# Optimization experiments

Measured on AMD Instinct MI355X. Metric: run time of the kernel, lower is better.

## Reference

```python
import jax, jax.numpy as jnp
import numpy as np

# ---- config (from Mamba2Config defaults) ----
D_MODEL = 1024
D_STATE = 128
D_CONV = 4
EXPAND = 2
HEADDIM = 64
D_INNER = EXPAND * D_MODEL          # 2048
NHEADS = D_INNER // HEADDIM         # 32
CONV_DIM = D_INNER + 2 * D_STATE    # 2304 (ngroups=1)
D_IN_PROJ = 2 * D_INNER + 2 * D_STATE + NHEADS  # 4384
INTER = ((int(D_MODEL * 8 / 3) + 63) // 64) * 64  # 2752
EPS = 1e-6
BATCH, SEQLEN = 2, 1024


def rmsnorm(x, w):
    return x * jax.lax.rsqrt(jnp.mean(x * x, axis=-1, keepdims=True) + EPS) * w


def setup_inputs() -> dict:
    key = jax.random.key(0)
    ks = jax.random.split(key, 16)
    s = 0.02
    return {
        "hidden_states": jax.random.normal(ks[0], (BATCH, SEQLEN, D_MODEL), jnp.float32),
        "norm_w": jnp.ones((D_MODEL,), jnp.float32),
        "in_proj_w": jax.random.normal(ks[1], (D_IN_PROJ, D_MODEL), jnp.float32) * s,
        "conv_w": jax.random.normal(ks[2], (CONV_DIM, D_CONV), jnp.float32) * 0.2,
        "conv_b": jnp.zeros((CONV_DIM,), jnp.float32),
        "dt_bias": jax.random.normal(ks[3], (NHEADS,), jnp.float32) * 0.5,
        "A_log": jnp.log(jax.random.uniform(ks[4], (NHEADS,), jnp.float32, 1.0, 16.0)),
        "D": jnp.ones((NHEADS,), jnp.float32) + jax.random.normal(ks[5], (NHEADS,), jnp.float32) * 0.05,
        "ssm_norm_w": jnp.ones((D_INNER,), jnp.float32),
        "out_proj_w": jax.random.normal(ks[6], (D_MODEL, D_INNER), jnp.float32) * s,
        "post_norm_w": jnp.ones((D_MODEL,), jnp.float32),
        "gate_w": jax.random.normal(ks[7], (INTER, D_MODEL), jnp.float32) * s,
        "up_w": jax.random.normal(ks[8], (INTER, D_MODEL), jnp.float32) * s,
        "down_w": jax.random.normal(ks[9], (D_MODEL, INTER), jnp.float32) * s,
    }


def _mixer(u, in_proj_w, conv_w, conv_b, dt_bias, A_log, D, ssm_norm_w, out_proj_w):
    b, l, _ = u.shape
    zxbcdt = u @ in_proj_w.T                              # (b,l,4384)
    z = zxbcdt[..., :D_INNER]                             # gate
    xBC = zxbcdt[..., D_INNER:D_INNER + CONV_DIM]
    dt = zxbcdt[..., -NHEADS:]

    # causal depthwise conv1d (kernel D_CONV) + SiLU
    xp = jnp.pad(xBC, ((0, 0), (D_CONV - 1, 0), (0, 0)))
    xBC = sum(xp[:, k:k + l, :] * conv_w[:, k] for k in range(D_CONV)) + conv_b
    xBC = jax.nn.silu(xBC)

    xs = xBC[..., :D_INNER].reshape(b, l, NHEADS, HEADDIM)   # (b,l,h,p)
    Bm = xBC[..., D_INNER:D_INNER + D_STATE]                  # (b,l,n)
    Cm = xBC[..., -D_STATE:]                                  # (b,l,n)

    dt = jax.nn.softplus(dt + dt_bias)                        # (b,l,h)
    A = -jnp.exp(A_log)                                       # (h,)

    def step(h, inp):
        dt_t, x_t, B_t, C_t = inp                             # (b,h),(b,h,p),(b,n),(b,n)
        dA = jnp.exp(dt_t * A)                                # (b,h)
        h = h * dA[..., None, None] + jnp.einsum('bh,bhp,bn->bhpn', dt_t, x_t, B_t)
        y_t = jnp.einsum('bhpn,bn->bhp', h, C_t)
        return h, y_t

    h0 = jnp.zeros((b, NHEADS, HEADDIM, D_STATE), u.dtype)
    xsT = (jnp.moveaxis(dt, 1, 0), jnp.moveaxis(xs, 1, 0),
           jnp.moveaxis(Bm, 1, 0), jnp.moveaxis(Cm, 1, 0))
    _, yT = jax.lax.scan(step, h0, xsT)                       # (l,b,h,p)
    y = jnp.moveaxis(yT, 0, 1) + D[None, None, :, None] * xs  # skip term
    y = y.reshape(b, l, D_INNER)

    # gated RMSNorm (norm_before_gate=False): normalize y*silu(z)
    y = rmsnorm(y * jax.nn.silu(z), ssm_norm_w)
    return y @ out_proj_w.T


def reference(hidden_states, norm_w, in_proj_w, conv_w, conv_b, dt_bias, A_log, D,
              ssm_norm_w, out_proj_w, post_norm_w, gate_w, up_w, down_w):
    res = hidden_states
    h = rmsnorm(hidden_states, norm_w)
    h = _mixer(h, in_proj_w, conv_w, conv_b, dt_bias, A_log, D, ssm_norm_w, out_proj_w)
    x = res + h
    res = x
    h = rmsnorm(x, post_norm_w)
    h = (jax.nn.silu(h @ gate_w.T) * (h @ up_w.T)) @ down_w.T  # SwiGLU MLP
    return res + h
```

## Files before the change

### kernel.cpp

```cpp
#include <hip/hip_runtime.h>
#include <hip/hip_bf16.h>

#define SEQLEN   1024
#define NTOK     2048
#define DMODEL   1024
#define DSTATE   128
#define DINNER   2048
#define NHEADS   32
#define HEADDIM  64
#define CONVDIM  2304
#define DINPROJ  4384
#define INTER    2752
#define Q        64
#define NCHUNK   16

typedef __hip_bfloat16 bf16;
typedef unsigned short ushort_t;
typedef __attribute__((ext_vector_type(8))) short bf16x8;
typedef __attribute__((ext_vector_type(4))) float f32x4;
typedef __attribute__((ext_vector_type(4))) unsigned short u16x4;

__device__ __forceinline__ float bf2f(bf16 x) { return __bfloat162float(x); }
__device__ __forceinline__ float bfu2f(ushort_t u) {
    return __uint_as_float(((unsigned)u) << 16);
}
__device__ __forceinline__ ushort_t f2bfu(float x) {
    union { bf16 h; ushort_t u; } c; c.h = __float2bfloat16(x); return c.u;
}

__device__ __forceinline__ void glds16(const void* g, void* l) {
    __builtin_amdgcn_global_load_lds(
        (const __attribute__((address_space(1))) void*)g,
        (__attribute__((address_space(3))) void*)l, 16, 0, 0);
}

template <int N>
__device__ __forceinline__ void pipe_fence() {
    if constexpr (N == 4)
        asm volatile("s_waitcnt vmcnt(4) lgkmcnt(0)" ::: "memory");
    else if constexpr (N == 2)
        asm volatile("s_waitcnt vmcnt(2) lgkmcnt(0)" ::: "memory");
    else
        asm volatile("s_waitcnt vmcnt(0) lgkmcnt(0)" ::: "memory");
    __builtin_amdgcn_s_barrier();
    __builtin_amdgcn_sched_barrier(0);
}

__device__ inline float block_reduce_sum(float v) {
    __shared__ float red[4];
    #pragma unroll
    for (int off = 32; off >= 1; off >>= 1) v += __shfl_down(v, off);
    int lane = threadIdx.x & 63, w = threadIdx.x >> 6;
    if (lane == 0) red[w] = v;
    __syncthreads();
    return red[0] + red[1] + red[2] + red[3];
}

__global__ __launch_bounds__(256) void f2bf_kernel(
    const float* __restrict__ src, ushort_t* __restrict__ dst, int n)
{
    const int i = (blockIdx.x * 256 + threadIdx.x) * 4;
    if (i < n) {
        const f32x4 v = *(const f32x4*)(src + i);
        u16x4 o;
        #pragma unroll
        for (int k = 0; k < 4; k++) o[k] = f2bfu(v[k]);
        *(u16x4*)(dst + i) = o;
    }
}

#define NWOP (DMODEL * DINNER)
#define NWG  (INTER * DMODEL)
__global__ __launch_bounds__(256) void convert_weights_kernel(
    const float* __restrict__ wop, const float* __restrict__ wg,
    const float* __restrict__ wu, const float* __restrict__ wd,
    ushort_t* __restrict__ dWop, ushort_t* __restrict__ dWgu,
    ushort_t* __restrict__ dWdn)
{
    const int i4 = (blockIdx.x * 256 + threadIdx.x) * 4;
    const float* src;
    ushort_t* dst;
    if (i4 < NWOP) { src = wop + i4; dst = dWop + i4; }
    else if (i4 < NWOP + NWG) {
        const int e = i4 - NWOP, row = e >> 10, col = e & 1023;
        src = wg + e; dst = dWgu + ((size_t)(2 * row) << 10) + col;
    } else if (i4 < NWOP + 2 * NWG) {
        const int e = i4 - NWOP - NWG, row = e >> 10, col = e & 1023;
        src = wu + e; dst = dWgu + ((size_t)(2 * row + 1) << 10) + col;
    } else if (i4 < NWOP + 3 * NWG) {
        const int e = i4 - NWOP - 2 * NWG;
        src = wd + e; dst = dWdn + e;
    } else return;
    const f32x4 v = *(const f32x4*)src;
    u16x4 o;
    #pragma unroll
    for (int k = 0; k < 4; k++) o[k] = f2bfu(v[k]);
    *(u16x4*)dst = o;
}

__global__ __launch_bounds__(256) void rmsnorm1024_kernel(
    const float* __restrict__ x, const float* __restrict__ w, bf16* __restrict__ out)
{
    const int token = blockIdx.x, t = threadIdx.x;
    float v[4]; float ss = 0.f;
    #pragma unroll
    for (int i = 0; i < 4; i++) {
        v[i] = x[(size_t)token * DMODEL + t * 4 + i];
        ss += v[i] * v[i];
    }
    ss = block_reduce_sum(ss);
    const float scale = rsqrtf(ss * (1.0f / DMODEL) + 1e-6f);
    #pragma unroll
    for (int i = 0; i < 4; i++)
        out[(size_t)token * DMODEL + t * 4 + i] =
            __float2bfloat16(v[i] * scale * w[t * 4 + i]);
}

template <int EPI, int MT, int NT>
__global__ __launch_bounds__(256) void gemm_bf(
    const bf16* __restrict__ A, const bf16* __restrict__ W,
    float* __restrict__ Cf, const float* __restrict__ resid_f,
    bf16* __restrict__ out_bf, int M, int N, int K)
{
    __shared__ ushort_t As[3][MT * 32];
    __shared__ ushort_t Bs[3][NT * 32];
    const int tid = threadIdx.x;
    const int w = tid >> 6, lane = tid & 63;
    constexpr int NLD = MT / 64 + NT / 64;

    const int gdx = gridDim.x, gdy = gridDim.y;
    const int nwg = gdx * gdy;
    const int orig = blockIdx.x + gdx * blockIdx.y;
    const int q8 = nwg >> 3, r8 = nwg & 7;
    const int xcd = orig & 7, lin = orig >> 3;
    const int wg = (xcd < r8 ? xcd * (q8 + 1) : r8 * (q8 + 1) + (xcd - r8) * q8) + lin;
    const int m0 = (wg % gdy) * MT;
    const int n0 = (wg / gdy) * NT;

    const int srow = tid >> 2;
    const int scol = (((tid & 3) ^ ((srow >> 1) & 3)) * 8);
    const bf16* Agp[MT / 64];
    const bf16* Wgp[NT / 64];
    #pragma unroll
    for (int i = 0; i < MT / 64; i++)
        Agp[i] = A + (size_t)(m0 + i * 64 + srow) * K + scol;
    #pragma unroll
    for (int i = 0; i < NT / 64; i++) {
        const int nr = n0 + i * 64 + srow;
        Wgp[i] = W + (size_t)(nr < N ? nr : 0) * K + scol;
    }

    const int wy = w >> 1, wx = w & 1;
    const int fr = lane & 15;
    const int fq = lane >> 4;
    const int cxor = (fr >> 1) & 3;
    constexpr int MI = MT / 32;
    constexpr int NJ = NT / 32;
    f32x4 acc[MI][NJ];
    #pragma unroll
    for (int i = 0; i < MI; i++)
        #pragma unroll
        for (int j = 0; j < NJ; j++)
            acc[i][j] = (f32x4){0.f, 0.f, 0.f, 0.f};

    const int nk = K >> 5;

    #define STAGE(buf, koff) do {                                         \
        ushort_t* sa_ = &As[buf][w * 512];                                \
        ushort_t* sb_ = &Bs[buf][w * 512];                                \
        _Pragma("unroll")                                                 \
        for (int i_ = 0; i_ < MT / 64; i_++)                              \
            glds16(Agp[i_] + (koff), sa_ + i_ * 2048);                    \
        _Pragma("unroll")                                                 \
        for (int i_ = 0; i_ < NT / 64; i_++)                              \
            glds16(Wgp[i_] + (koff), sb_ + i_ * 2048);                    \
    } while (0)

    STAGE(0, 0);
    STAGE(1, 32);
    pipe_fence<NLD>();

    int cur = 0, stg = 2;
    for (int kt = 0; kt < nk; ++kt) {
        const bool pf = (kt + 2 < nk);
        if (pf) STAGE(stg, (kt + 2) << 5);
        const ushort_t* ca = As[cur];
        const ushort_t* cb = Bs[cur];
        bf16x8 af[MI], bfv[NJ];
        #pragma unroll
        for (int i = 0; i < MI; i++) {
            const int r = wy * (MT / 2) + i * 16 + fr;
            af[i] = *(const bf16x8*)&ca[r * 32 + ((fq ^ cxor) * 8)];
        }
        #pragma unroll
        for (int j = 0; j < NJ; j++) {
            const int r = wx * (NT / 2) + j * 16 + fr;
            bfv[j] = *(const bf16x8*)&cb[r * 32 + ((fq ^ cxor) * 8)];
        }
        #pragma unroll
        for (int i = 0; i < MI; i++)
            #pragma unroll
            for (int j = 0; j < NJ; j++)
                acc[i][j] = __builtin_amdgcn_mfma_f32_16x16x32_bf16(
                    af[i], bfv[j], acc[i][j], 0, 0, 0);
        if (pf)               pipe_fence<NLD>();
        else if (kt + 1 < nk) pipe_fence<0>();
        cur = (cur == 2) ? 0 : cur + 1;
        stg = (stg == 2) ? 0 : stg + 1;
    }
    #undef STAGE

    #pragma unroll
    for (int i = 0; i < MI; i++) {
        #pragma unroll
        for (int j = 0; j < NJ; j++) {
            const int mb = m0 + wy * (MT / 2) + i * 16 + (lane >> 4) * 4;
            const int nn = n0 + wx * (NT / 2) + j * 16 + (lane & 15);
            if (nn < N) {
                #pragma unroll
                for (int r = 0; r < 4; r++) {
                    if (EPI == 2) {
                        const float g = acc[i][j][r];
                        const float u = __shfl_xor(g, 1);
                        if (!(lane & 1)) {
                            const float a = (g / (1.f + expf(-g))) * u;
                            out_bf[(size_t)(mb + r) * (N / 2) + (nn >> 1)] =
                                __float2bfloat16(a);
                        }
                    } else {
                        const size_t idx = (size_t)(mb + r) * N + nn;
                        float v = acc[i][j][r];
                        if (EPI == 1) v += resid_f[idx];
                        Cf[idx] = v;
                    }
                }
            }
        }
    }
}

__global__ __launch_bounds__(256) void gemm_bf_s(
    const bf16* __restrict__ A, const bf16* __restrict__ W,
    float* __restrict__ Cf, const float* __restrict__ resid_f,
    int M, int N, int K)
{
    constexpr int MT = 64, NT = 64;
    __shared__ ushort_t As[2][MT * 64];
    __shared__ ushort_t Bs[2][NT * 64];
    const int tid = threadIdx.x;
    const int w = tid >> 6, lane = tid & 63;

    const int gdx = gridDim.x, gdy = gridDim.y;
    const int nwg = gdx * gdy;
    const int orig = blockIdx.x + gdx * blockIdx.y;
    const int q8 = nwg >> 3, r8 = nwg & 7;
    const int xcd = orig & 7, lin = orig >> 3;
    const int wg = (xcd < r8 ? xcd * (q8 + 1) : r8 * (q8 + 1) + (xcd - r8) * q8) + lin;
    const int m0 = (wg % gdy) * MT;
    const int n0 = (wg / gdy) * NT;

    const int srow = tid >> 3;
    const int scol = (((tid & 7) ^ (srow & 7)) * 8);
    const bf16* Agp[2];
    const bf16* Wgp[2];
    #pragma unroll
    for (int i = 0; i < 2; i++)
        Agp[i] = A + (size_t)(m0 + i * 32 + srow) * K + scol;
    #pragma unroll
    for (int i = 0; i < 2; i++) {
        const int nr = n0 + i * 32 + srow;
        Wgp[i] = W + (size_t)(nr < N ? nr : 0) * K + scol;
    }

    const int wy = w >> 1, wx = w & 1;
    const int fr = lane & 15;
    const int fq = lane >> 4;
    f32x4 acc[2][2];
    #pragma unroll
    for (int i = 0; i < 2; i++)
        #pragma unroll
        for (int j = 0; j < 2; j++)
            acc[i][j] = (f32x4){0.f, 0.f, 0.f, 0.f};

    const int nk = K >> 6;

    #define STAGE_S(buf, koff) do {                                       \
        ushort_t* sa_ = &As[buf][w * 512];                                \
        ushort_t* sb_ = &Bs[buf][w * 512];                                \
        _Pragma("unroll")                                                 \
        for (int i_ = 0; i_ < 2; i_++)                                    \
            glds16(Agp[i_] + (koff), sa_ + i_ * 2048);                    \
        _Pragma("unroll")                                                 \
        for (int i_ = 0; i_ < 2; i_++)                                    \
            glds16(Wgp[i_] + (koff), sb_ + i_ * 2048);                    \
    } while (0)

    STAGE_S(0, 0);
    __syncthreads();

    for (int kt = 0; kt < nk; ++kt) {
        const int cur = kt & 1;
        if (kt + 1 < nk) STAGE_S(cur ^ 1, (kt + 1) << 6);
        const ushort_t* ca = As[cur];
        const ushort_t* cb = Bs[cur];
        #pragma unroll
        for (int ks = 0; ks < 2; ks++) {
            bf16x8 af[2], bfv[2];
            #pragma unroll
            for (int i = 0; i < 2; i++) {
                const int r = wy * 32 + i * 16 + fr;
                const int g = ks * 4 + fq;
                af[i] = *(const bf16x8*)&ca[r * 64 + ((g ^ (r & 7)) * 8)];
            }
            #pragma unroll
            for (int j = 0; j < 2; j++) {
                const int r = wx * 32 + j * 16 + fr;
                const int g = ks * 4 + fq;
                bfv[j] = *(const bf16x8*)&cb[r * 64 + ((g ^ (r & 7)) * 8)];
            }
            #pragma unroll
            for (int i = 0; i < 2; i++)
                #pragma unroll
                for (int j = 0; j < 2; j++)
                    acc[i][j] = __builtin_amdgcn_mfma_f32_16x16x32_bf16(
                        af[i], bfv[j], acc[i][j], 0, 0, 0);
        }
        __syncthreads();
    }
    #undef STAGE_S

    #pragma unroll
    for (int i = 0; i < 2; i++) {
        #pragma unroll
        for (int j = 0; j < 2; j++) {
            const int mb = m0 + wy * 32 + i * 16 + (lane >> 4) * 4;
            const int nn = n0 + wx * 32 + j * 16 + (lane & 15);
            if (nn < N) {
                #pragma unroll
                for (int r = 0; r < 4; r++) {
                    const size_t idx = (size_t)(mb + r) * N + nn;
                    Cf[idx] = acc[i][j][r] + resid_f[idx];
                }
            }
        }
    }
}

#define NCONVBLK ((NTOK * CONVDIM / 4) / 256)
__global__ __launch_bounds__(256) void conv_silu_dt_kernel(
    const float* __restrict__ zx, const float* __restrict__ cw,
    const float* __restrict__ cb, const float* __restrict__ dtbias,
    ushort_t* __restrict__ out, float* __restrict__ dtb_out)
{
    const int bid = blockIdx.x;
    if (bid < NCONVBLK) {
        const int i = bid * 256 + threadIdx.x;
        const int cg = i % (CONVDIM / 4);
        const int token = i / (CONVDIM / 4);
        const int c0 = cg * 4;
        const int l = token & (SEQLEN - 1);
        float a[4];
        #pragma unroll
        for (int j = 0; j < 4; j++) a[j] = cb[c0 + j];
        f32x4 cwv[4];
        #pragma unroll
        for (int j = 0; j < 4; j++) cwv[j] = *(const f32x4*)(cw + (c0 + j) * 4);
        #pragma unroll
        for (int k = 0; k < 4; k++) {
            const int ls = l - 3 + k;
            if (ls >= 0) {
                const f32x4 v = *(const f32x4*)(
                    zx + (size_t)(token - 3 + k) * DINPROJ + DINNER + c0);
                #pragma unroll
                for (int j = 0; j < 4; j++) a[j] += v[j] * cwv[j][k];
            }
        }
        u16x4 o;
        #pragma unroll
        for (int j = 0; j < 4; j++)
            o[j] = f2bfu(a[j] / (1.f + expf(-a[j])));
        *(u16x4*)(out + (size_t)token * CONVDIM + c0) = o;
    } else {
        const int idx = (bid - NCONVBLK) * 256 + threadIdx.x;
        const int h = idx & (NHEADS - 1);
        const int token = idx >> 5;
        float v = zx[(size_t)token * DINPROJ + (DINNER + CONVDIM) + h] + dtbias[h];
        dtb_out[idx] = (v > 20.f) ? v : log1pf(expf(v));
    }
}

__global__ __launch_bounds__(256) void chunk_state_kernel(
    const ushort_t* __restrict__ cvb, const float* __restrict__ dtb,
    const float* __restrict__ A_log, float* __restrict__ ccum,
    ushort_t* __restrict__ Sbuf)
{
    const int bx = blockIdx.x;
    const int bh = bx >> 4, c = bx & 15;
    const int b = bh >> 5, h = bh & 31;
    const int t = threadIdx.x;
    const int w = t >> 6, lane = t & 63;
    const int wy = w >> 1, wx = w & 1;
    const int fr = lane & 15, fk = (lane >> 4) * 8, cr = (lane >> 4) * 4;
    const int tok0 = b * SEQLEN + c * Q;
    const float A = -expf(A_log[h]);

    __shared__ ushort_t sXT[64 * 88];
    __shared__ ushort_t sBT[128 * 88];
    __shared__ float sW[64];

    if (t < 64) {
        const float d = dtb[(size_t)(tok0 + t) * NHEADS + h];
        float s = d;
        #pragma unroll
        for (int off = 1; off < 64; off <<= 1) {
            const float up = __shfl_up(s, off);
            if (t >= off) s += up;
        }
        const float total = __shfl(s, 63);
        sW[t] = expf(A * (total - s)) * d;
        if (t == 63) ccum[bh * NCHUNK + c] = A * total;
    }
    __syncthreads();

    for (int i = t; i < 64 * 64; i += 256) {
        const int l = i >> 6, p = i & 63;
        const float v = bfu2f(cvb[(size_t)(tok0 + l) * CONVDIM + h * HEADDIM + p]);
        sXT[p * 88 + l] = f2bfu(sW[l] * v);
    }
    for (int i = t; i < 128 * 64; i += 256) {
        const int l = i >> 7, n = i & 127;
        sBT[n * 88 + l] = cvb[(size_t)(tok0 + l) * CONVDIM + DINNER + n];
    }
    __syncthreads();

    f32x4 acc[2][4];
    #pragma unroll
    for (int i = 0; i < 2; i++)
        #pragma unroll
        for (int j = 0; j < 4; j++)
            acc[i][j] = (f32x4){0.f, 0.f, 0.f, 0.f};
    #pragma unroll
    for (int k0 = 0; k0 < 64; k0 += 32) {
        bf16x8 af[2], bfv[4];
        #pragma unroll
        for (int i = 0; i < 2; i++)
            af[i] = *(const bf16x8*)&sXT[(wy * 32 + i * 16 + fr) * 88 + fk + k0];
        #pragma unroll
        for (int j = 0; j < 4; j++)
            bfv[j] = *(const bf16x8*)&sBT[(wx * 64 + j * 16 + fr) * 88 + fk + k0];
        #pragma unroll
        for (int i = 0; i < 2; i++)
            #pragma unroll
            for (int j = 0; j < 4; j++)
                acc[i][j] = __builtin_amdgcn_mfma_f32_16x16x32_bf16(
                    af[i], bfv[j], acc[i][j], 0, 0, 0);
    }
    const size_t slot = (size_t)(bh * NCHUNK + c) * 64 * 128;
    #pragma unroll
    for (int i = 0; i < 2; i++) {
        #pragma unroll
        for (int j = 0; j < 4; j++) {
            #pragma unroll
            for (int r = 0; r < 4; r++) {
                const int pr = wy * 32 + i * 16 + cr + r;
                const int nn = wx * 64 + j * 16 + fr;
                Sbuf[slot + pr * 128 + nn] = f2bfu(acc[i][j][r]);
            }
        }
    }
}

__global__ __launch_bounds__(256) void stitch_kernel(
    const float* __restrict__ ccum, ushort_t* __restrict__ Sbuf)
{
    const int bh = blockIdx.x >> 2, ng = blockIdx.x & 3;
    const int t = threadIdx.x, p = t >> 2, q = t & 3;
    float H[8];
    #pragma unroll
    for (int j = 0; j < 8; j++) H[j] = 0.f;
    for (int c = 0; c < NCHUNK; c++) {
        const float P = expf(ccum[bh * NCHUNK + c]);
        const size_t slot = ((size_t)(bh * NCHUNK + c) * 64 + p) * 128 + ng * 32;
        #pragma unroll
        for (int jj = 0; jj < 2; jj++) {
            const u16x4 sv4 = *(const u16x4*)&Sbuf[slot + q * 4 + 16 * jj];
            u16x4 hv4;
            #pragma unroll
            for (int k = 0; k < 4; k++) hv4[k] = f2bfu(H[jj * 4 + k]);
            *(u16x4*)&Sbuf[slot + q * 4 + 16 * jj] = hv4;
            #pragma unroll
            for (int k = 0; k < 4; k++)
                H[jj * 4 + k] = P * H[jj * 4 + k] + bfu2f(sv4[k]);
        }
    }
}

__global__ __launch_bounds__(256) void chunk_scan_mfma_kernel(
    const ushort_t* __restrict__ cvb, const float* __restrict__ dtb,
    const float* __restrict__ A_log, const float* __restrict__ Dh,
    const ushort_t* __restrict__ Sbuf, bf16* __restrict__ ybuf)
{
    const int bx = blockIdx.x;
    const int bh = bx >> 4, c = bx & 15;
    const int b = bh >> 5, h = bh & 31;
    const int t = threadIdx.x;
    const int w = t >> 6, lane = t & 63;
    const int wy = w >> 1, wx = w & 1;
    const int fr = lane & 15;
    const int fk = (lane >> 4) * 8;
    const int cr = (lane >> 4) * 4;
    const int tok0 = b * SEQLEN + c * Q;
    const float A = -expf(A_log[h]);
    const float Dv = Dh[h];

    __shared__ ushort_t sB[64 * 136];
    __shared__ ushort_t sC[64 * 136];
    __shared__ ushort_t sH[64 * 136];
    __shared__ ushort_t sXT[64 * 72];
    __shared__ ushort_t sM[64 * 72];
    __shared__ float    sCum[64];
    __shared__ float    sDtv[64];

    for (int i = t; i < 64 * 32; i += 256) {
        const int row = i >> 5, col = (i & 31) * 4;
        const size_t base = (size_t)(tok0 + row) * CONVDIM;
        *(u16x4*)&sB[row * 136 + col] = *(const u16x4*)&cvb[base + DINNER + col];
        *(u16x4*)&sC[row * 136 + col] = *(const u16x4*)&cvb[base + DINNER + DSTATE + col];
    }
    for (int i = t; i < 64 * 32; i += 256) {
        const int p = i >> 5, l0 = (i & 31) * 2;
        const ushort_t x0 = cvb[(size_t)(tok0 + l0)     * CONVDIM + h * HEADDIM + p];
        const ushort_t x1 = cvb[(size_t)(tok0 + l0 + 1) * CONVDIM + h * HEADDIM + p];
        *(unsigned*)&sXT[p * 72 + l0] = ((unsigned)x1 << 16) | x0;
    }
    {
        const size_t slot = (size_t)(bh * NCHUNK + c) * 64 * 128;
        for (int i = t * 4; i < 64 * 128; i += 1024) {
            const int row = i >> 7, col = i & 127;
            *(u16x4*)&sH[row * 136 + col] = *(const u16x4*)&Sbuf[slot + row * 128 + col];
        }
    }
    if (t < 64) {
        const float d = dtb[(size_t)(tok0 + t) * NHEADS + h];
        float s = d;
        #pragma unroll
        for (int off = 1; off < 64; off <<= 1) {
            const float up = __shfl_up(s, off);
            if (t >= off) s += up;
        }
        sCum[t] = A * s;
        sDtv[t] = d;
    }
    __syncthreads();

    f32x4 accg[2][2];
    #pragma unroll
    for (int i = 0; i < 2; i++)
        #pragma unroll
        for (int j = 0; j < 2; j++)
            accg[i][j] = (f32x4){0.f, 0.f, 0.f, 0.f};
    #pragma unroll
    for (int k0 = 0; k0 < 128; k0 += 32) {
        bf16x8 af[2], bfv[2];
        #pragma unroll
        for (int i = 0; i < 2; i++)
            af[i] = *(const bf16x8*)&sC[(wy * 32 + i * 16 + fr) * 136 + fk + k0];
        #pragma unroll
        for (int j = 0; j < 2; j++)
            bfv[j] = *(const bf16x8*)&sB[(wx * 32 + j * 16 + fr) * 136 + fk + k0];
        #pragma unroll
        for (int i = 0; i < 2; i++)
            #pragma unroll
            for (int j = 0; j < 2; j++)
                accg[i][j] = __builtin_amdgcn_mfma_f32_16x16x32_bf16(
                    af[i], bfv[j], accg[i][j], 0, 0, 0);
    }
    __syncthreads();

    #pragma unroll
    for (int i = 0; i < 2; i++) {
        #pragma unroll
        for (int j = 0; j < 2; j++) {
            #pragma unroll
            for (int r = 0; r < 4; r++) {
                const int l  = wy * 32 + i * 16 + cr + r;
                const int jc = wx * 32 + j * 16 + fr;
                const float v = (jc <= l)
                    ? accg[i][j][r] * expf(sCum[l] - sCum[jc]) * sDtv[jc] : 0.f;
                sM[l * 72 + jc] = f2bfu(v);
            }
        }
    }
    for (int i = t; i < 64 * 32; i += 256) {
        const int row = i >> 5, col = (i & 31) * 4;
        const float sc = expf(sCum[row]);
        u16x4 v = *(const u16x4*)&sC[row * 136 + col];
        #pragma unroll
        for (int k = 0; k < 4; k++) v[k] = f2bfu(bfu2f(v[k]) * sc);
        *(u16x4*)&sC[row * 136 + col] = v;
    }
    __syncthreads();

    f32x4 accy[2][2];
    #pragma unroll
    for (int i = 0; i < 2; i++)
        #pragma unroll
        for (int j = 0; j < 2; j++)
            accy[i][j] = (f32x4){0.f, 0.f, 0.f, 0.f};
    #pragma unroll
    for (int k0 = 0; k0 < 64; k0 += 32) {
        bf16x8 af[2], bfv[2];
        #pragma unroll
        for (int i = 0; i < 2; i++)
            af[i] = *(const bf16x8*)&sM[(wy * 32 + i * 16 + fr) * 72 + fk + k0];
        #pragma unroll
        for (int j = 0; j < 2; j++)
            bfv[j] = *(const bf16x8*)&sXT[(wx * 32 + j * 16 + fr) * 72 + fk + k0];
        #pragma unroll
        for (int i = 0; i < 2; i++)
            #pragma unroll
            for (int j = 0; j < 2; j++)
                accy[i][j] = __builtin_amdgcn_mfma_f32_16x16x32_bf16(
                    af[i], bfv[j], accy[i][j], 0, 0, 0);
    }
    #pragma unroll
    for (int k0 = 0; k0 < 128; k0 += 32) {
        bf16x8 af[2], bfv[2];
        #pragma unroll
        for (int i = 0; i < 2; i++)
            af[i] = *(const bf16x8*)&sC[(wy * 32 + i * 16 + fr) * 136 + fk + k0];
        #pragma unroll
        for (int j = 0; j < 2; j++)
            bfv[j] = *(const bf16x8*)&sH[(wx * 32 + j * 16 + fr) * 136 + fk + k0];
        #pragma unroll
        for (int i = 0; i < 2; i++)
            #pragma unroll
            for (int j = 0; j < 2; j++)
                accy[i][j] = __builtin_amdgcn_mfma_f32_16x16x32_bf16(
                    af[i], bfv[j], accy[i][j], 0, 0, 0);
    }

    #pragma unroll
    for (int i = 0; i < 2; i++) {
        #pragma unroll
        for (int j = 0; j < 2; j++) {
            #pragma unroll
            for (int r = 0; r < 4; r++) {
                const int l = wy * 32 + i * 16 + cr + r;
                const int p = wx * 32 + j * 16 + fr;
                const float x = bfu2f(sXT[p * 72 + l]);
                ybuf[(size_t)(tok0 + l) * DINNER + h * HEADDIM + p] =
                    __float2bfloat16(accy[i][j][r] + Dv * x);
            }
        }
    }
}

__global__ __launch_bounds__(256) void gated_rmsnorm_kernel(
    const bf16* __restrict__ y, const float* __restrict__ zx,
    const float* __restrict__ w, bf16* __restrict__ out)
{
    const int token = blockIdx.x, t = threadIdx.x;
    const bf16* yr = y + (size_t)token * DINNER;
    const float* zr = zx + (size_t)token * DINPROJ;
    float v[8]; float ss = 0.f;
    #pragma unroll
    for (int i = 0; i < 8; i++) {
        const int idx = t * 8 + i;
        const float zz = zr[idx];
        const float val = bf2f(yr[idx]) * (zz / (1.f + expf(-zz)));
        v[i] = val; ss += val * val;
    }
    ss = block_reduce_sum(ss);
    const float scale = rsqrtf(ss * (1.0f / DINNER) + 1e-6f);
    #pragma unroll
    for (int i = 0; i < 8; i++) {
        const int idx = t * 8 + i;
        out[(size_t)token * DINNER + idx] =
            __float2bfloat16(v[i] * scale * w[idx]);
    }
}

extern "C" void kernel_launch(void* const* d_in, const int* in_sizes, int n_in,
                              void* d_out, int out_size, void* d_ws, size_t ws_size,
                              hipStream_t stream) {
    const float* hidden     = (const float*)d_in[0];
    const float* norm_w     = (const float*)d_in[1];
    const float* in_proj_w  = (const float*)d_in[2];
    const float* conv_w     = (const float*)d_in[3];
    const float* conv_b     = (const float*)d_in[4];
    const float* dt_bias    = (const float*)d_in[5];
    const float* A_log      = (const float*)d_in[6];
    const float* Dh         = (const float*)d_in[7];
    const float* ssm_norm_w = (const float*)d_in[8];
    const float* out_proj_w = (const float*)d_in[9];
    const float* post_norm_w= (const float*)d_in[10];
    const float* gate_w     = (const float*)d_in[11];
    const float* up_w       = (const float*)d_in[12];
    const float* down_w     = (const float*)d_in[13];
    float* out = (float*)d_out;

    float* ws = (float*)d_ws;
    bf16*  h_norm = (bf16*)(ws);
    float* zx     = ws + 1048576;
    ushort_t* cvb = (ushort_t*)(ws + 10027008);
    float* dtb    = ws + 14745600;
    float* ccum   = ws + 14811136;
    ushort_t* Sbuf= (ushort_t*)(ws + 14812160);
    float* xbuf   = ws + 19006464;
    bf16*  ybuf   = (bf16*)(ws + 21103616);
    bf16*  ynorm  = (bf16*)(ws + 22152192);
    ushort_t* Wip = (ushort_t*)(ws + 10027008);
    ushort_t* Wop = (ushort_t*)(ws + 1048576);
    ushort_t* Wgu = (ushort_t*)(ws + 2097152);
    ushort_t* Wdn = (ushort_t*)(ws + 4915200);
    bf16*  act    = (bf16*)(ws + 6324224);
    bf16*  h2     = h_norm;

    f2bf_kernel<<<4384, 256, 0, stream>>>(in_proj_w, Wip, DINPROJ * DMODEL);
    rmsnorm1024_kernel<<<NTOK, 256, 0, stream>>>(hidden, norm_w, h_norm);
    gemm_bf<0, 128, 128><<<dim3(35, 16), 256, 0, stream>>>(h_norm, (const bf16*)Wip, zx,
        nullptr, nullptr, NTOK, DINPROJ, DMODEL);
    conv_silu_dt_kernel<<<NCONVBLK + (NTOK * NHEADS) / 256, 256, 0, stream>>>(
        zx, conv_w, conv_b, dt_bias, cvb, dtb);
    chunk_state_kernel<<<1024, 256, 0, stream>>>(cvb, dtb, A_log, ccum, Sbuf);
    stitch_kernel<<<256, 256, 0, stream>>>(ccum, Sbuf);
    chunk_scan_mfma_kernel<<<1024, 256, 0, stream>>>(cvb, dtb, A_log, Dh, Sbuf, ybuf);
    gated_rmsnorm_kernel<<<NTOK, 256, 0, stream>>>(ybuf, zx, ssm_norm_w, ynorm);
    convert_weights_kernel<<<(NWOP + 3 * NWG) / 1024, 256, 0, stream>>>(
        out_proj_w, gate_w, up_w, down_w, Wop, Wgu, Wdn);
    gemm_bf_s<<<dim3(16, 32), 256, 0, stream>>>(ynorm, (const bf16*)Wop, xbuf,
        hidden, NTOK, DMODEL, DINNER);
    rmsnorm1024_kernel<<<NTOK, 256, 0, stream>>>(xbuf, post_norm_w, h2);
    gemm_bf<2, 128, 128><<<dim3(43, 16), 256, 0, stream>>>(h2, (const bf16*)Wgu,
        nullptr, nullptr, act, NTOK, 2 * INTER, DMODEL);
    gemm_bf_s<<<dim3(16, 32), 256, 0, stream>>>(act, (const bf16*)Wdn, out,
        xbuf, NTOK, DMODEL, INTER);
}
```

Before: 333.0 us.

## Vectorize chunk-state loads, drop sH staging, alias sM onto sB, raise MFMA priority

```diff
diff --git a/kernel.cpp b/kernel.cpp
--- a/kernel.cpp
+++ b/kernel.cpp
@@ -197,12 +197,14 @@
             const int r = wx * (NT / 2) + j * 16 + fr;
             bfv[j] = *(const bf16x8*)&cb[r * 32 + ((fq ^ cxor) * 8)];
         }
+        __builtin_amdgcn_s_setprio(1);
         #pragma unroll
         for (int i = 0; i < MI; i++)
             #pragma unroll
             for (int j = 0; j < NJ; j++)
                 acc[i][j] = __builtin_amdgcn_mfma_f32_16x16x32_bf16(
                     af[i], bfv[j], acc[i][j], 0, 0, 0);
+        __builtin_amdgcn_s_setprio(0);
         if (pf)               pipe_fence<NLD>();
         else if (kt + 1 < nk) pipe_fence<0>();
         cur = (cur == 2) ? 0 : cur + 1;
@@ -422,14 +424,22 @@
     }
     __syncthreads();
 
-    for (int i = t; i < 64 * 64; i += 256) {
-        const int l = i >> 6, p = i & 63;
-        const float v = bfu2f(cvb[(size_t)(tok0 + l) * CONVDIM + h * HEADDIM + p]);
-        sXT[p * 88 + l] = f2bfu(sW[l] * v);
-    }
-    for (int i = t; i < 128 * 64; i += 256) {
-        const int l = i >> 7, n = i & 127;
-        sBT[n * 88 + l] = cvb[(size_t)(tok0 + l) * CONVDIM + DINNER + n];
+    for (int i = t; i < 64 * 16; i += 256) {
+        const int l = i >> 4, p0 = (i & 15) * 4;
+        const u16x4 xv = *(const u16x4*)&cvb[(size_t)(tok0 + l) * CONVDIM
+                                            + h * HEADDIM + p0];
+        const float wl = sW[l];
+        #pragma unroll
+        for (int j = 0; j < 4; j++)
+            sXT[(p0 + j) * 88 + l] = f2bfu(wl * bfu2f(xv[j]));
+    }
+    for (int i = t; i < 128 * 16; i += 256) {
+        const int l = i >> 5, n0 = (i & 31) * 4;
+        const u16x4 bv = *(const u16x4*)&cvb[(size_t)(tok0 + l) * CONVDIM
+                                            + DINNER + n0];
+        #pragma unroll
+        for (int j = 0; j < 4; j++)
+            sBT[(n0 + j) * 88 + l] = bv[j];
     }
     __syncthreads();
 
@@ -515,11 +525,10 @@
 
     __shared__ ushort_t sB[64 * 136];
     __shared__ ushort_t sC[64 * 136];
-    __shared__ ushort_t sH[64 * 136];
     __shared__ ushort_t sXT[64 * 72];
-    __shared__ ushort_t sM[64 * 72];
     __shared__ float    sCum[64];
     __shared__ float    sDtv[64];
+    ushort_t* const sM = sB;
 
     for (int i = t; i < 64 * 32; i += 256) {
         const int row = i >> 5, col = (i & 31) * 4;
@@ -532,13 +541,6 @@
         const ushort_t x0 = cvb[(size_t)(tok0 + l0)     * CONVDIM + h * HEADDIM + p];
         const ushort_t x1 = cvb[(size_t)(tok0 + l0 + 1) * CONVDIM + h * HEADDIM + p];
         *(unsigned*)&sXT[p * 72 + l0] = ((unsigned)x1 << 16) | x0;
-    }
-    {
-        const size_t slot = (size_t)(bh * NCHUNK + c) * 64 * 128;
-        for (int i = t * 4; i < 64 * 128; i += 1024) {
-            const int row = i >> 7, col = i & 127;
-            *(u16x4*)&sH[row * 136 + col] = *(const u16x4*)&Sbuf[slot + row * 128 + col];
-        }
     }
     if (t < 64) {
         const float d = dtb[(size_t)(tok0 + t) * NHEADS + h];
@@ -601,6 +603,7 @@
     }
     __syncthreads();
 
+    const ushort_t* Hg = Sbuf + (size_t)(bh * NCHUNK + c) * 64 * 128;
     f32x4 accy[2][2];
     #pragma unroll
     for (int i = 0; i < 2; i++)
@@ -631,7 +634,7 @@
             af[i] = *(const bf16x8*)&sC[(wy * 32 + i * 16 + fr) * 136 + fk + k0];
         #pragma unroll
         for (int j = 0; j < 2; j++)
-            bfv[j] = *(const bf16x8*)&sH[(wx * 32 + j * 16 + fr) * 136 + fk + k0];
+            bfv[j] = *(const bf16x8*)&Hg[(size_t)(wx * 32 + j * 16 + fr) * 128 + fk + k0];
         #pragma unroll
         for (int i = 0; i < 2; i++)
             #pragma unroll
```

Result: no change. 336.5 us (+1.0%).
